# Performance work log

Hardware: AMD Instinct MI355X
Metric: run time of the kernel (lower is better)

## Reference

```python
import jax, jax.numpy as jnp
import numpy as np

B, T, C, H = 8, 1024, 768, 12
D = C // H  # head dim = 64


def setup_inputs() -> dict:
    key = jax.random.key(0)
    ks = jax.random.split(key, 5)
    x = jax.random.normal(ks[0], (B, T, C), dtype=jnp.float32)
    W_attn = jax.random.normal(ks[1], (C, 3 * C), dtype=jnp.float32) * 0.02
    b_attn = jnp.zeros((3 * C,), dtype=jnp.float32)
    W_proj = jax.random.normal(ks[2], (C, C), dtype=jnp.float32) * 0.02
    b_proj = jnp.zeros((C,), dtype=jnp.float32)
    return {"x": x, "W_attn": W_attn, "b_attn": b_attn, "W_proj": W_proj, "b_proj": b_proj}


def reference(x, W_attn, b_attn, W_proj, b_proj):
    Bx, Tx, Cx = x.shape
    qkv = x @ W_attn + b_attn                      # [B,T,3C]
    q, k, v = jnp.split(qkv, 3, axis=-1)           # each [B,T,C]
    # [B,T,C] -> [B,H,T,D]
    q = q.reshape(Bx, Tx, H, D).transpose(0, 2, 1, 3)
    k = k.reshape(Bx, Tx, H, D).transpose(0, 2, 1, 3)
    v = v.reshape(Bx, Tx, H, D).transpose(0, 2, 1, 3)
    scale = 1.0 / jnp.sqrt(jnp.asarray(D, dtype=x.dtype))
    att = jnp.einsum('bhqd,bhkd->bhqk', q, k) * scale   # [B,H,T,T]
    causal = jnp.tril(jnp.ones((Tx, Tx), dtype=bool))    # [T,T]
    att = jnp.where(causal[None, None, :, :], att, jnp.asarray(-jnp.inf, dtype=att.dtype))
    att = jax.nn.softmax(att, axis=-1)
    y = jnp.einsum('bhqk,bhkd->bhqd', att, v)            # [B,H,T,D]
    y = y.transpose(0, 2, 1, 3).reshape(Bx, Tx, Cx)      # [B,T,C]
    return y @ W_proj + b_proj
```

## Files before the change

### kernel.cpp

```cpp
#include <hip/hip_runtime.h>
#include <stdint.h>

typedef short short8 __attribute__((ext_vector_type(8)));
typedef float f32x4 __attribute__((ext_vector_type(4)));

__device__ __forceinline__ unsigned short f2bf(float f) {
    union { float f; uint32_t u; } v; v.f = f;
    uint32_t u = v.u;
    u += 0x7FFFu + ((u >> 16) & 1u);
    return (unsigned short)(u >> 16);
}

__device__ __forceinline__ uint32_t cvtpk(float lo, float hi) {
    uint32_t r;
    asm("v_cvt_pk_bf16_f32 %0, %1, %2" : "=v"(r) : "v"(lo), "v"(hi));
    return r;
}

__device__ __forceinline__ void gload_lds16(const void* g, void* l) {
    __builtin_amdgcn_global_load_lds(
        (const __attribute__((address_space(1))) void*)g,
        (__attribute__((address_space(3))) void*)l, 16, 0, 0);
}

__device__ __forceinline__ void transpose_body(const float* __restrict__ in,
                                               unsigned short* __restrict__ out,
                                               int R, int Cc, int bx, int by,
                                               float (*tile)[33]) {
    int c0 = bx * 32, r0 = by * 32;
    int tr = threadIdx.x / 32, c = threadIdx.x % 32;
#pragma unroll
    for (int rr = tr; rr < 32; rr += 8)
        tile[rr][c] = in[(size_t)(r0 + rr) * Cc + c0 + c];
    __syncthreads();
#pragma unroll
    for (int rr = tr; rr < 32; rr += 8)
        out[(size_t)(c0 + rr) * R + r0 + c] = f2bf(tile[c][rr]);
}

__global__ void k_prep(const float* __restrict__ x, unsigned short* __restrict__ xb,
                       const float* __restrict__ Wa, unsigned short* __restrict__ WaT,
                       const float* __restrict__ Wp, unsigned short* __restrict__ WpT) {
    __shared__ float tile[32][33];
    const int blk = blockIdx.x;
    if (blk < 3072) {
#pragma unroll
        for (int j = 0; j < 2; ++j) {
            int i = blk * 512 + j * 256 + threadIdx.x;
            float4 f = ((const float4*)x)[i];
            ushort4 o;
            o.x = f2bf(f.x); o.y = f2bf(f.y); o.z = f2bf(f.z); o.w = f2bf(f.w);
            ((ushort4*)xb)[i] = o;
        }
    } else if (blk < 3072 + 1728) {
        int id = blk - 3072;
        transpose_body(Wa, WaT, 768, 2304, id % 72, id / 72, tile);
    } else {
        int id = blk - 4800;
        transpose_body(Wp, WpT, 768, 768, id % 24, id / 24, tile);
    }
}

template<bool F32OUT, bool VSPLIT, int NFRAG>
__global__ __launch_bounds__(256, 3)
void k_gemm_bt(const unsigned short* __restrict__ A, const unsigned short* __restrict__ BT,
               const float* __restrict__ bias, void* __restrict__ Cout,
               unsigned short* __restrict__ Vt,
               int M, int N, int K) {
    __shared__ unsigned short As[2][128][32];
    __shared__ unsigned short Bs[2][NFRAG * 32][32];
    const int nbx = gridDim.x;
    const int total = nbx * gridDim.y;
    const int id = blockIdx.y * nbx + blockIdx.x;
    int m_, n_;
    if (VSPLIT) {
        const int x = id & 7, j = id >> 3;
        const int panel = j / 48, jj = j % 48;
        m_ = x * 8 + (jj & 7);
        n_ = panel * 6 + (jj >> 3);
    } else {
        const int sw = (id & 7) * (total >> 3) + (id >> 3);
        m_ = sw / nbx;
        n_ = sw % nbx;
    }
    const int m0 = m_ * 128, n0 = n_ * (NFRAG * 32);
    const int t = threadIdx.x;
    const int w = t >> 6, l = t & 63;
    const int wm = (w >> 1) * 64, wn = (w & 1) * (NFRAG * 16);
    const int lr = l & 15, lg = l >> 4;
    const int srow = w * 32 + (l >> 2);
    const int srowB = (NFRAG == 4) ? srow : (w * 16 + (l >> 2));
    const int scol = (l & 3) * 8;
    const unsigned short* pa = &A [(size_t)(m0 + srow)  * K + scol];
    const unsigned short* pb = &BT[(size_t)(n0 + srowB) * K + scol];

    f32x4 acc[4][NFRAG];
#pragma unroll
    for (int i = 0; i < 4; ++i)
#pragma unroll
        for (int j = 0; j < NFRAG; ++j)
#pragma unroll
            for (int r = 0; r < 4; ++r) acc[i][j][r] = 0.0f;

    for (int k0 = 0; k0 < K; k0 += 64) {
        __syncthreads();
        gload_lds16(pa + k0,                        &As[0][w * 32][0]);
        gload_lds16(pa + (size_t)16 * K + k0,       &As[0][w * 32 + 16][0]);
        gload_lds16(pa + k0 + 32,                   &As[1][w * 32][0]);
        gload_lds16(pa + (size_t)16 * K + k0 + 32,  &As[1][w * 32 + 16][0]);
        if (NFRAG == 4) {
            gload_lds16(pb + k0,                        &Bs[0][w * 32][0]);
            gload_lds16(pb + (size_t)16 * K + k0,       &Bs[0][w * 32 + 16][0]);
            gload_lds16(pb + k0 + 32,                   &Bs[1][w * 32][0]);
            gload_lds16(pb + (size_t)16 * K + k0 + 32,  &Bs[1][w * 32 + 16][0]);
        } else {
            gload_lds16(pb + k0,                        &Bs[0][w * 16][0]);
            gload_lds16(pb + k0 + 32,                   &Bs[1][w * 16][0]);
        }
        __syncthreads();
#pragma unroll
        for (int p = 0; p < 2; ++p) {
            short8 af[4], bfv[NFRAG];
#pragma unroll
            for (int f = 0; f < 4; ++f)
                af[f] = *(const short8*)&As[p][wm + f * 16 + lr][lg * 8];
#pragma unroll
            for (int f = 0; f < NFRAG; ++f)
                bfv[f] = *(const short8*)&Bs[p][wn + f * 16 + lr][lg * 8];
#pragma unroll
            for (int mf = 0; mf < 4; ++mf)
#pragma unroll
                for (int nf = 0; nf < NFRAG; ++nf)
                    acc[mf][nf] = __builtin_amdgcn_mfma_f32_16x16x32_bf16(af[mf], bfv[nf], acc[mf][nf], 0, 0, 0);
        }
    }

#pragma unroll
    for (int mf = 0; mf < 4; ++mf)
#pragma unroll
        for (int nf = 0; nf < NFRAG; ++nf) {
            int n = n0 + wn + nf * 16 + lr;
            int mbase = m0 + wm + mf * 16 + lg * 4;
            float bv = bias[n];
            if (VSPLIT && n >= 1536) {
                int hh = (n - 1536) >> 6, dd = (n - 1536) & 63;
                int bb = mbase >> 10, tt = mbase & 1023;
                ushort4 o;
                o.x = f2bf(acc[mf][nf][0] + bv);
                o.y = f2bf(acc[mf][nf][1] + bv);
                o.z = f2bf(acc[mf][nf][2] + bv);
                o.w = f2bf(acc[mf][nf][3] + bv);
                *(ushort4*)&Vt[(((size_t)bb * 12 + hh) * 64 + dd) * 1024 + tt] = o;
            } else {
#pragma unroll
                for (int r = 0; r < 4; ++r) {
                    float v = acc[mf][nf][r] + bv;
                    if (F32OUT) ((float*)Cout)[(size_t)(mbase + r) * N + n] = v;
                    else ((unsigned short*)Cout)[(size_t)(mbase + r) * N + n] = f2bf(v);
                }
            }
        }
}

__global__ __launch_bounds__(256, 3)
void k_attn(const unsigned short* __restrict__ qkv, const unsigned short* __restrict__ vt,
            unsigned short* __restrict__ y) {
    __shared__ unsigned short Ks[64][88];
    __shared__ unsigned short Vs[64][88];
    __shared__ unsigned short Ps[4][16][72];
    const int p = blockIdx.x;
    const int s = p >> 3;
    const int bh = (p & 7) * 12 + (s >> 3);
    const int qt = 7 - ((s + 3 * (s >> 5)) & 7);
    const int b = bh / 12, h = bh % 12;
    const int t = threadIdx.x, w = t >> 6, l = t & 63, lr = l & 15, lg = l >> 4;
    const int q0 = qt * 128;

    const unsigned short* qbase = qkv + (size_t)b * 1024 * 2304 + h * 64;
    const unsigned short* kbase = qbase + 768;
    const unsigned short* vbase = vt + (size_t)bh * 64 * 1024;

    const int srow = t >> 2, scol = (t & 3) * 8;
    const unsigned short* kst = &kbase[(size_t)srow * 2304 + scol];
    const unsigned short* vst = &vbase[(size_t)srow * 1024 + scol];

    short8 qf[2][2];
#pragma unroll
    for (int g = 0; g < 2; ++g) {
        const unsigned short* qrow = &qbase[(size_t)(q0 + g * 64 + w * 16 + lr) * 2304];
        qf[g][0] = *(const short8*)&qrow[lg * 8];
        qf[g][1] = *(const short8*)&qrow[32 + lg * 8];
    }

    float l_loc[2] = {0.0f, 0.0f};
    f32x4 o_acc[2][4];
#pragma unroll
    for (int g = 0; g < 2; ++g)
#pragma unroll
        for (int df = 0; df < 4; ++df)
#pragma unroll
            for (int r = 0; r < 4; ++r) o_acc[g][df][r] = 0.0f;

    {
        uint4 ka = *(const uint4*)(kst);
        uint4 kb = *(const uint4*)(kst + 32);
        uint4 va = *(const uint4*)(vst);
        uint4 vb = *(const uint4*)(vst + 32);
        *(uint4*)&Ks[srow][scol]      = ka;
        *(uint4*)&Ks[srow][scol + 32] = kb;
        *(uint4*)&Vs[srow][scol]      = va;
        *(uint4*)&Vs[srow][scol + 32] = vb;
    }
    __syncthreads();

    const int nkt = qt * 2 + 2;
    for (int kti = 0; kti < nkt; ++kti) {
        const int kt = kti * 64;
        const bool more = (kti + 1 < nkt);
        uint4 nka, nkb, nva, nvb;
        if (more) {
            const int kn = kt + 64;
            nka = *(const uint4*)(kst + (size_t)kn * 2304);
            nkb = *(const uint4*)(kst + (size_t)kn * 2304 + 32);
            nva = *(const uint4*)(vst + kn);
            nvb = *(const uint4*)(vst + kn + 32);
        }

        const bool act0 = (kti < nkt - 1);
        const bool dg0  = (kti == nkt - 2);
        const bool dg1  = (kti == nkt - 1);

        f32x4 s0[4], s1[4];
        __builtin_amdgcn_s_setprio(1);
#pragma unroll
        for (int nf = 0; nf < 4; ++nf) {
            short8 kf0 = *(const short8*)&Ks[nf * 16 + lr][lg * 8];
            short8 kf1 = *(const short8*)&Ks[nf * 16 + lr][32 + lg * 8];
            f32x4 z0, z1;
#pragma unroll
            for (int r = 0; r < 4; ++r) { z0[r] = 0.0f; z1[r] = 0.0f; }
            if (act0 && (!dg0 || nf <= w)) {
                z0 = __builtin_amdgcn_mfma_f32_16x16x32_bf16(kf0, qf[0][0], z0, 0, 0, 0);
                z0 = __builtin_amdgcn_mfma_f32_16x16x32_bf16(kf1, qf[0][1], z0, 0, 0, 0);
            }
            if (!dg1 || nf <= w) {
                z1 = __builtin_amdgcn_mfma_f32_16x16x32_bf16(kf0, qf[1][0], z1, 0, 0, 0);
                z1 = __builtin_amdgcn_mfma_f32_16x16x32_bf16(kf1, qf[1][1], z1, 0, 0, 0);
            }
            s0[nf] = z0; s1[nf] = z1;
        }
        __builtin_amdgcn_s_setprio(0);

        short8 vf[4][2];
#pragma unroll
        for (int df = 0; df < 4; ++df) {
            vf[df][0] = *(const short8*)&Vs[df * 16 + lr][lg * 8];
            vf[df][1] = *(const short8*)&Vs[df * 16 + lr][32 + lg * 8];
        }

#pragma unroll
        for (int g = 0; g < 2; ++g) {
            if (g == 0 && !act0) continue;
            const bool diag = g ? dg1 : dg0;
            const int row = q0 + g * 64 + w * 16 + lr;
            float lsum = 0.0f;
#pragma unroll
            for (int nf = 0; nf < 4; ++nf) {
                float e[4];
#pragma unroll
                for (int r = 0; r < 4; ++r) {
                    int col = kt + nf * 16 + lg * 4 + r;
                    bool ok = !diag || (nf < w) || (col <= row);
                    float sv = g ? s1[nf][r] : s0[nf][r];
                    e[r] = ok ? __builtin_amdgcn_exp2f(fmaf(sv, 0.18033688f, -11.54156003f)) : 0.0f;
                    lsum += e[r];
                }
                uint2 u;
                u.x = cvtpk(e[0], e[1]);
                u.y = cvtpk(e[2], e[3]);
                *(uint2*)&Ps[w][lr][nf * 16 + lg * 4] = u;
            }
            l_loc[g] += lsum;
            short8 pf0 = *(const short8*)&Ps[w][lr][lg * 8];
            short8 pf1 = *(const short8*)&Ps[w][lr][32 + lg * 8];
            __builtin_amdgcn_s_setprio(1);
#pragma unroll
            for (int df = 0; df < 4; ++df) {
                o_acc[g][df] = __builtin_amdgcn_mfma_f32_16x16x32_bf16(pf0, vf[df][0], o_acc[g][df], 0, 0, 0);
                o_acc[g][df] = __builtin_amdgcn_mfma_f32_16x16x32_bf16(pf1, vf[df][1], o_acc[g][df], 0, 0, 0);
            }
            __builtin_amdgcn_s_setprio(0);
        }

        if (more) {
            __syncthreads();
            *(uint4*)&Ks[srow][scol]      = nka;
            *(uint4*)&Ks[srow][scol + 32] = nkb;
            *(uint4*)&Vs[srow][scol]      = nva;
            *(uint4*)&Vs[srow][scol + 32] = nvb;
            __syncthreads();
        }
    }

#pragma unroll
    for (int g = 0; g < 2; ++g) {
        float dsum = l_loc[g];
        dsum += __shfl_xor(dsum, 16);
        dsum += __shfl_xor(dsum, 32);
#pragma unroll
        for (int r = 0; r < 4; ++r) {
            float inv = 1.0f / __shfl(dsum, lg * 4 + r);
            int rowy = q0 + g * 64 + w * 16 + lg * 4 + r;
#pragma unroll
            for (int df = 0; df < 4; ++df)
                y[((size_t)b * 1024 + rowy) * 768 + h * 64 + df * 16 + lr] = f2bf(o_acc[g][df][r] * inv);
        }
    }
}

extern "C" void kernel_launch(void* const* d_in, const int* in_sizes, int n_in,
                              void* d_out, int out_size, void* d_ws, size_t ws_size,
                              hipStream_t stream) {
    const float* x  = (const float*)d_in[0];
    const float* Wa = (const float*)d_in[1];
    const float* ba = (const float*)d_in[2];
    const float* Wp = (const float*)d_in[3];
    const float* bp = (const float*)d_in[4];
    float* out = (float*)d_out;

    char* ws = (char*)d_ws;
    unsigned short* qkv = (unsigned short*)ws;
    unsigned short* xb  = (unsigned short*)(ws + 37748736);
    unsigned short* WaT = (unsigned short*)(ws + 37748736 + 12582912);
    unsigned short* WpT = (unsigned short*)(ws + 37748736 + 12582912 + 3538944);
    unsigned short* y   = xb;
    unsigned short* vtb = (unsigned short*)d_out;

    k_prep<<<5376, 256, 0, stream>>>(x, xb, Wa, WaT, Wp, WpT);
    k_gemm_bt<false, true, 4><<<dim3(18, 64), 256, 0, stream>>>(xb, WaT, ba, qkv, vtb, 8192, 2304, 768);
    k_attn<<<768, 256, 0, stream>>>(qkv, vtb, y);
    k_gemm_bt<true, false, 2><<<dim3(12, 64), 256, 0, stream>>>(y, WpT, bp, out, nullptr, 8192, 768, 768);
}
```

Measured before the change: 102.7 us.

## Double-buffer 32-wide K/V tiles in attention with per-warp causal skipping

Shrinks the attention key tile from 64 to 32 columns and double-buffers the K and V tiles in LDS, which removes one of the two barriers per iteration. Causal skipping becomes per warp at 16-column granularity, so less masked MFMA and exp work runs near the diagonal. In exchange there are twice as many loop iterations, each with a barrier and less MFMA work to hide latency. LDS use per block also drops.

```diff
diff --git a/kernel.cpp b/kernel.cpp
--- a/kernel.cpp
+++ b/kernel.cpp
@@ -165,9 +165,9 @@
 __global__ __launch_bounds__(256, 3)
 void k_attn(const unsigned short* __restrict__ qkv, const unsigned short* __restrict__ vt,
             unsigned short* __restrict__ y) {
-    __shared__ unsigned short Ks[64][88];
-    __shared__ unsigned short Vs[64][88];
-    __shared__ unsigned short Ps[4][16][72];
+    __shared__ unsigned short Ks[2][32][72];
+    __shared__ unsigned short Vs[2][64][40];
+    __shared__ unsigned short Ps[4][16][40];
     const int p = blockIdx.x;
     const int s = p >> 3;
     const int bh = (p & 7) * 12 + (s >> 3);
@@ -180,14 +180,18 @@
     const unsigned short* kbase = qbase + 768;
     const unsigned short* vbase = vt + (size_t)bh * 64 * 1024;
 
-    const int srow = t >> 2, scol = (t & 3) * 8;
-    const unsigned short* kst = &kbase[(size_t)srow * 2304 + scol];
-    const unsigned short* vst = &vbase[(size_t)srow * 1024 + scol];
+    const int krow = t >> 3, kcol = (t & 7) * 8;
+    const int drow = t >> 2, vcol = (t & 3) * 8;
+    const unsigned short* kst = &kbase[(size_t)krow * 2304 + kcol];
+    const unsigned short* vst = &vbase[(size_t)drow * 1024 + vcol];
+
+    const int rowb0 = q0 + w * 16;
+    const int rowb1 = q0 + 64 + w * 16;
 
     short8 qf[2][2];
 #pragma unroll
     for (int g = 0; g < 2; ++g) {
-        const unsigned short* qrow = &qbase[(size_t)(q0 + g * 64 + w * 16 + lr) * 2304];
+        const unsigned short* qrow = &qbase[(size_t)((g ? rowb1 : rowb0) + lr) * 2304];
         qf[g][0] = *(const short8*)&qrow[lg * 8];
         qf[g][1] = *(const short8*)&qrow[32 + lg * 8];
     }
@@ -201,49 +205,35 @@
 #pragma unroll
             for (int r = 0; r < 4; ++r) o_acc[g][df][r] = 0.0f;
 
-    {
-        uint4 ka = *(const uint4*)(kst);
-        uint4 kb = *(const uint4*)(kst + 32);
-        uint4 va = *(const uint4*)(vst);
-        uint4 vb = *(const uint4*)(vst + 32);
-        *(uint4*)&Ks[srow][scol]      = ka;
-        *(uint4*)&Ks[srow][scol + 32] = kb;
-        *(uint4*)&Vs[srow][scol]      = va;
-        *(uint4*)&Vs[srow][scol + 32] = vb;
-    }
+    *(uint4*)&Ks[0][krow][kcol] = *(const uint4*)(kst);
+    *(uint4*)&Vs[0][drow][vcol] = *(const uint4*)(vst);
     __syncthreads();
 
-    const int nkt = qt * 2 + 2;
+    const int nkt = qt * 4 + 4;
+    int cur = 0;
     for (int kti = 0; kti < nkt; ++kti) {
-        const int kt = kti * 64;
+        const int kt = kti * 32;
         const bool more = (kti + 1 < nkt);
-        uint4 nka, nkb, nva, nvb;
+        uint4 nk, nv;
         if (more) {
-            const int kn = kt + 64;
-            nka = *(const uint4*)(kst + (size_t)kn * 2304);
-            nkb = *(const uint4*)(kst + (size_t)kn * 2304 + 32);
-            nva = *(const uint4*)(vst + kn);
-            nvb = *(const uint4*)(vst + kn + 32);
-        }
-
-        const bool act0 = (kti < nkt - 1);
-        const bool dg0  = (kti == nkt - 2);
-        const bool dg1  = (kti == nkt - 1);
-
-        f32x4 s0[4], s1[4];
+            nk = *(const uint4*)(kst + (size_t)(kt + 32) * 2304);
+            nv = *(const uint4*)(vst + kt + 32);
+        }
+
+        f32x4 s0[2], s1[2];
         __builtin_amdgcn_s_setprio(1);
 #pragma unroll
-        for (int nf = 0; nf < 4; ++nf) {
-            short8 kf0 = *(const short8*)&Ks[nf * 16 + lr][lg * 8];
-            short8 kf1 = *(const short8*)&Ks[nf * 16 + lr][32 + lg * 8];
+        for (int nf = 0; nf < 2; ++nf) {
+            short8 kf0 = *(const short8*)&Ks[cur][nf * 16 + lr][lg * 8];
+            short8 kf1 = *(const short8*)&Ks[cur][nf * 16 + lr][32 + lg * 8];
             f32x4 z0, z1;
 #pragma unroll
             for (int r = 0; r < 4; ++r) { z0[r] = 0.0f; z1[r] = 0.0f; }
-            if (act0 && (!dg0 || nf <= w)) {
+            if (kt + nf * 16 <= rowb0 + 15) {
                 z0 = __builtin_amdgcn_mfma_f32_16x16x32_bf16(kf0, qf[0][0], z0, 0, 0, 0);
                 z0 = __builtin_amdgcn_mfma_f32_16x16x32_bf16(kf1, qf[0][1], z0, 0, 0, 0);
             }
-            if (!dg1 || nf <= w) {
+            if (kt + nf * 16 <= rowb1 + 15) {
                 z1 = __builtin_amdgcn_mfma_f32_16x16x32_bf16(kf0, qf[1][0], z1, 0, 0, 0);
                 z1 = __builtin_amdgcn_mfma_f32_16x16x32_bf16(kf1, qf[1][1], z1, 0, 0, 0);
             }
@@ -251,28 +241,25 @@
         }
         __builtin_amdgcn_s_setprio(0);
 
-        short8 vf[4][2];
-#pragma unroll
-        for (int df = 0; df < 4; ++df) {
-            vf[df][0] = *(const short8*)&Vs[df * 16 + lr][lg * 8];
-            vf[df][1] = *(const short8*)&Vs[df * 16 + lr][32 + lg * 8];
-        }
+        short8 vf[4];
+#pragma unroll
+        for (int df = 0; df < 4; ++df)
+            vf[df] = *(const short8*)&Vs[cur][df * 16 + lr][lg * 8];
 
 #pragma unroll
         for (int g = 0; g < 2; ++g) {
-            if (g == 0 && !act0) continue;
-            const bool diag = g ? dg1 : dg0;
-            const int row = q0 + g * 64 + w * 16 + lr;
+            const int rowb = g ? rowb1 : rowb0;
+            if (kt > rowb + 15) continue;
+            const int row = rowb + lr;
             float lsum = 0.0f;
 #pragma unroll
-            for (int nf = 0; nf < 4; ++nf) {
+            for (int nf = 0; nf < 2; ++nf) {
                 float e[4];
 #pragma unroll
                 for (int r = 0; r < 4; ++r) {
                     int col = kt + nf * 16 + lg * 4 + r;
-                    bool ok = !diag || (nf < w) || (col <= row);
                     float sv = g ? s1[nf][r] : s0[nf][r];
-                    e[r] = ok ? __builtin_amdgcn_exp2f(fmaf(sv, 0.18033688f, -11.54156003f)) : 0.0f;
+                    e[r] = (col <= row) ? __builtin_amdgcn_exp2f(fmaf(sv, 0.18033688f, -11.54156003f)) : 0.0f;
                     lsum += e[r];
                 }
                 uint2 u;
@@ -281,25 +268,20 @@
                 *(uint2*)&Ps[w][lr][nf * 16 + lg * 4] = u;
             }
             l_loc[g] += lsum;
-            short8 pf0 = *(const short8*)&Ps[w][lr][lg * 8];
-            short8 pf1 = *(const short8*)&Ps[w][lr][32 + lg * 8];
+            short8 pf = *(const short8*)&Ps[w][lr][lg * 8];
             __builtin_amdgcn_s_setprio(1);
 #pragma unroll
-            for (int df = 0; df < 4; ++df) {
-                o_acc[g][df] = __builtin_amdgcn_mfma_f32_16x16x32_bf16(pf0, vf[df][0], o_acc[g][df], 0, 0, 0);
-                o_acc[g][df] = __builtin_amdgcn_mfma_f32_16x16x32_bf16(pf1, vf[df][1], o_acc[g][df], 0, 0, 0);
-            }
+            for (int df = 0; df < 4; ++df)
+                o_acc[g][df] = __builtin_amdgcn_mfma_f32_16x16x32_bf16(pf, vf[df], o_acc[g][df], 0, 0, 0);
             __builtin_amdgcn_s_setprio(0);
         }
 
         if (more) {
-            __syncthreads();
-            *(uint4*)&Ks[srow][scol]      = nka;
-            *(uint4*)&Ks[srow][scol + 32] = nkb;
-            *(uint4*)&Vs[srow][scol]      = nva;
-            *(uint4*)&Vs[srow][scol + 32] = nvb;
-            __syncthreads();
-        }
+            *(uint4*)&Ks[cur ^ 1][krow][kcol] = nk;
+            *(uint4*)&Vs[cur ^ 1][drow][vcol] = nv;
+        }
+        __syncthreads();
+        cur ^= 1;
     }
 
 #pragma unroll
@@ -310,7 +292,7 @@
 #pragma unroll
         for (int r = 0; r < 4; ++r) {
             float inv = 1.0f / __shfl(dsum, lg * 4 + r);
-            int rowy = q0 + g * 64 + w * 16 + lg * 4 + r;
+            int rowy = (g ? rowb1 : rowb0) + lg * 4 + r;
 #pragma unroll
             for (int df = 0; df < 4; ++df)
                 y[((size_t)b * 1024 + rowy) * 768 + h * 64 + df * 16 + lr] = f2bf(o_acc[g][df][r] * inv);
```

After: 106.6 us. 1.04x slower.
